# Kernel tuning notes

Hardware: AMD Instinct MI355X
Metric: run time of the kernel (lower is better)

Reference implementation:

```python
import jax, jax.numpy as jnp
import numpy as np

VOCAB = 30522
HIDDEN = 768
MAX_POS = 512
TYPE_VOCAB = 2
EPS = 1e-5


def setup_inputs() -> dict:
    key = jax.random.key(0)
    k1, k2, k3, k4, k5 = jax.random.split(key, 5)
    B, S = 32, 512
    return {
        "input_ids": jax.random.randint(k1, (B, S), 0, VOCAB, dtype=jnp.int64 if jax.config.jax_enable_x64 else jnp.int32),
        "token_type_ids": jax.random.randint(k2, (B, S), 0, TYPE_VOCAB, dtype=jnp.int32),
        "tok_w": jax.random.normal(k3, (VOCAB, HIDDEN), dtype=jnp.float32),
        "pos_w": jax.random.normal(k4, (MAX_POS, HIDDEN), dtype=jnp.float32),
        "type_w": jax.random.normal(k5, (TYPE_VOCAB, HIDDEN), dtype=jnp.float32),
        "gamma": jnp.ones((HIDDEN,), dtype=jnp.float32),
        "beta": jnp.zeros((HIDDEN,), dtype=jnp.float32),
    }


def reference(input_ids, token_type_ids, tok_w, pos_w, type_w, gamma, beta):
    S = input_ids.shape[-1]
    # One-hot-matmul lookups are mathematically plain gathers.
    emb = tok_w[input_ids] + pos_w[jnp.arange(S)] + type_w[token_type_ids]  # [B,S,H]
    mean = jnp.mean(emb, axis=-1, keepdims=True)
    var = jnp.mean(jnp.square(emb - mean), axis=-1, keepdims=True)  # unbiased=False
    out = (emb - mean) * gamma * jax.lax.rsqrt(var + EPS) + beta
    return out  # dropout p=0.0 (eval) is identity
```

## Files before the change

kernel.cpp:

```cpp
#include <hip/hip_runtime.h>

#define HIDDEN 768
#define LN_EPS 1e-5f

typedef float f32x4 __attribute__((ext_vector_type(4)));

__global__ __launch_bounds__(256) void bert_embedding_kernel(
    const int* __restrict__ input_ids,
    const int* __restrict__ token_type_ids,
    const float* __restrict__ tok_w,
    const float* __restrict__ pos_w,
    const float* __restrict__ type_w,
    const float* __restrict__ gamma,
    const float* __restrict__ beta,
    float* __restrict__ out,
    int n_rows, int S)
{
    const int wave = (blockIdx.x * blockDim.x + threadIdx.x) >> 6;
    const int lane = threadIdx.x & 63;
    if (wave >= n_rows) return;

    const int s = wave % S;
    const int tok = input_ids[wave];
    const int typ = token_type_ids[wave];

    const f32x4* __restrict__ tw = reinterpret_cast<const f32x4*>(tok_w  + (size_t)tok * HIDDEN);
    const f32x4* __restrict__ pw = reinterpret_cast<const f32x4*>(pos_w  + (size_t)s   * HIDDEN);
    const f32x4* __restrict__ yw = reinterpret_cast<const f32x4*>(type_w + (size_t)typ * HIDDEN);

    f32x4 e[3];
    float sum = 0.f, sumsq = 0.f;
    #pragma unroll
    for (int k = 0; k < 3; ++k) {
        const int idx = lane + k * 64;
        const f32x4 a = tw[idx];
        const f32x4 b = pw[idx];
        const f32x4 c = yw[idx];
        f32x4 v = a + b + c;
        e[k] = v;
        sum   += v.x + v.y + v.z + v.w;
        sumsq += v.x * v.x + v.y * v.y + v.z * v.z + v.w * v.w;
    }

    #pragma unroll
    for (int m = 1; m < 64; m <<= 1) {
        sum   += __shfl_xor(sum, m);
        sumsq += __shfl_xor(sumsq, m);
    }

    const float inv_h = 1.0f / (float)HIDDEN;
    const float mean = sum * inv_h;
    const float var  = sumsq * inv_h - mean * mean;
    const float rs   = rsqrtf(var + LN_EPS);

    f32x4* __restrict__ o = reinterpret_cast<f32x4*>(out + (size_t)wave * HIDDEN);
    const f32x4* __restrict__ g4 = reinterpret_cast<const f32x4*>(gamma);
    const f32x4* __restrict__ b4 = reinterpret_cast<const f32x4*>(beta);

    #pragma unroll
    for (int k = 0; k < 3; ++k) {
        const int idx = lane + k * 64;
        const f32x4 g  = g4[idx];
        const f32x4 bb = b4[idx];
        const f32x4 v  = e[k];
        f32x4 r;
        r.x = (v.x - mean) * rs * g.x + bb.x;
        r.y = (v.y - mean) * rs * g.y + bb.y;
        r.z = (v.z - mean) * rs * g.z + bb.z;
        r.w = (v.w - mean) * rs * g.w + bb.w;
        __builtin_nontemporal_store(r, &o[idx]);
    }
}

extern "C" void kernel_launch(void* const* d_in, const int* in_sizes, int n_in,
                              void* d_out, int out_size, void* d_ws, size_t ws_size,
                              hipStream_t stream) {
    const int*   input_ids      = (const int*)d_in[0];
    const int*   token_type_ids = (const int*)d_in[1];
    const float* tok_w          = (const float*)d_in[2];
    const float* pos_w          = (const float*)d_in[3];
    const float* type_w         = (const float*)d_in[4];
    const float* gamma          = (const float*)d_in[5];
    const float* beta           = (const float*)d_in[6];
    float* out = (float*)d_out;

    const int n_rows = in_sizes[0];
    const int S = in_sizes[3] / HIDDEN;

    const int waves_per_block = 4;
    const int blocks = (n_rows + waves_per_block - 1) / waves_per_block;
    bert_embedding_kernel<<<blocks, 256, 0, stream>>>(
        input_ids, token_type_ids, tok_w, pos_w, type_w, gamma, beta,
        out, n_rows, S);
}
```

Measured before the change: 21.01 us.

## Use persistent grid-stride waves with double-buffered row prefetch

Switches from one wave per row to a capped grid of waves that walk rows in a grid-stride loop. Each wave loads the next row's token, position and type embeddings while it normalizes the current one, and gamma/beta are loaded once per wave and kept in registers. The aim is to hide gather latency and cut per-row setup cost. The price is higher register pressure from two sets of buffers, and lower occupancy or fewer rows in flight per CU than the launch-everything approach.

After: 21.95 us. 1.04x slower.

```diff
diff --git a/kernel.cpp b/kernel.cpp
--- a/kernel.cpp
+++ b/kernel.cpp
@@ -16,59 +16,83 @@
     float* __restrict__ out,
     int n_rows, int S)
 {
+    const int lane = threadIdx.x & 63;
     const int wave = (blockIdx.x * blockDim.x + threadIdx.x) >> 6;
-    const int lane = threadIdx.x & 63;
+    const int NW   = (gridDim.x * blockDim.x) >> 6;
     if (wave >= n_rows) return;
 
-    const int s = wave % S;
-    const int tok = input_ids[wave];
-    const int typ = token_type_ids[wave];
+    const int i0 = lane, i1 = lane + 64, i2 = lane + 128;
 
-    const f32x4* __restrict__ tw = reinterpret_cast<const f32x4*>(tok_w  + (size_t)tok * HIDDEN);
-    const f32x4* __restrict__ pw = reinterpret_cast<const f32x4*>(pos_w  + (size_t)s   * HIDDEN);
-    const f32x4* __restrict__ yw = reinterpret_cast<const f32x4*>(type_w + (size_t)typ * HIDDEN);
-
-    f32x4 e[3];
-    float sum = 0.f, sumsq = 0.f;
-    #pragma unroll
-    for (int k = 0; k < 3; ++k) {
-        const int idx = lane + k * 64;
-        const f32x4 a = tw[idx];
-        const f32x4 b = pw[idx];
-        const f32x4 c = yw[idx];
-        f32x4 v = a + b + c;
-        e[k] = v;
-        sum   += v.x + v.y + v.z + v.w;
-        sumsq += v.x * v.x + v.y * v.y + v.z * v.z + v.w * v.w;
-    }
-
-    #pragma unroll
-    for (int m = 1; m < 64; m <<= 1) {
-        sum   += __shfl_xor(sum, m);
-        sumsq += __shfl_xor(sumsq, m);
-    }
-
-    const float inv_h = 1.0f / (float)HIDDEN;
-    const float mean = sum * inv_h;
-    const float var  = sumsq * inv_h - mean * mean;
-    const float rs   = rsqrtf(var + LN_EPS);
-
-    f32x4* __restrict__ o = reinterpret_cast<f32x4*>(out + (size_t)wave * HIDDEN);
     const f32x4* __restrict__ g4 = reinterpret_cast<const f32x4*>(gamma);
     const f32x4* __restrict__ b4 = reinterpret_cast<const f32x4*>(beta);
+    const f32x4 g0 = g4[i0], g1 = g4[i1], g2 = g4[i2];
+    const f32x4 bb0 = b4[i0], bb1 = b4[i1], bb2 = b4[i2];
 
-    #pragma unroll
-    for (int k = 0; k < 3; ++k) {
-        const int idx = lane + k * 64;
-        const f32x4 g  = g4[idx];
-        const f32x4 bb = b4[idx];
-        const f32x4 v  = e[k];
-        f32x4 r;
-        r.x = (v.x - mean) * rs * g.x + bb.x;
-        r.y = (v.y - mean) * rs * g.y + bb.y;
-        r.z = (v.z - mean) * rs * g.z + bb.z;
-        r.w = (v.w - mean) * rs * g.w + bb.w;
-        __builtin_nontemporal_store(r, &o[idx]);
+    auto LOAD = [&](int r, f32x4* a, f32x4* p, f32x4* c) {
+        const int tok = input_ids[r];
+        const int typ = token_type_ids[r];
+        const int s   = r % S;
+        const f32x4* __restrict__ tw = reinterpret_cast<const f32x4*>(tok_w  + (size_t)tok * HIDDEN);
+        const f32x4* __restrict__ pw = reinterpret_cast<const f32x4*>(pos_w  + (size_t)s   * HIDDEN);
+        const f32x4* __restrict__ yw = reinterpret_cast<const f32x4*>(type_w + (size_t)typ * HIDDEN);
+        a[0] = tw[i0]; a[1] = tw[i1]; a[2] = tw[i2];
+        p[0] = pw[i0]; p[1] = pw[i1]; p[2] = pw[i2];
+        c[0] = yw[i0]; c[1] = yw[i1]; c[2] = yw[i2];
+    };
+
+    auto PROCESS = [&](int r, const f32x4* a, const f32x4* p, const f32x4* c) {
+        const f32x4 e0 = a[0] + p[0] + c[0];
+        const f32x4 e1 = a[1] + p[1] + c[1];
+        const f32x4 e2 = a[2] + p[2] + c[2];
+        float sum = e0.x + e0.y + e0.z + e0.w
+                  + e1.x + e1.y + e1.z + e1.w
+                  + e2.x + e2.y + e2.z + e2.w;
+        float sq  = e0.x*e0.x + e0.y*e0.y + e0.z*e0.z + e0.w*e0.w
+                  + e1.x*e1.x + e1.y*e1.y + e1.z*e1.z + e1.w*e1.w
+                  + e2.x*e2.x + e2.y*e2.y + e2.z*e2.z + e2.w*e2.w;
+        #pragma unroll
+        for (int m = 1; m < 64; m <<= 1) {
+            sum += __shfl_xor(sum, m);
+            sq  += __shfl_xor(sq, m);
+        }
+        const float inv_h = 1.0f / (float)HIDDEN;
+        const float mean = sum * inv_h;
+        const float rs   = rsqrtf(sq * inv_h - mean * mean + LN_EPS);
+
+        f32x4* __restrict__ o = reinterpret_cast<f32x4*>(out + (size_t)r * HIDDEN);
+        f32x4 r0, r1, r2;
+        r0.x = (e0.x - mean) * rs * g0.x + bb0.x;
+        r0.y = (e0.y - mean) * rs * g0.y + bb0.y;
+        r0.z = (e0.z - mean) * rs * g0.z + bb0.z;
+        r0.w = (e0.w - mean) * rs * g0.w + bb0.w;
+        r1.x = (e1.x - mean) * rs * g1.x + bb1.x;
+        r1.y = (e1.y - mean) * rs * g1.y + bb1.y;
+        r1.z = (e1.z - mean) * rs * g1.z + bb1.z;
+        r1.w = (e1.w - mean) * rs * g1.w + bb1.w;
+        r2.x = (e2.x - mean) * rs * g2.x + bb2.x;
+        r2.y = (e2.y - mean) * rs * g2.y + bb2.y;
+        r2.z = (e2.z - mean) * rs * g2.z + bb2.z;
+        r2.w = (e2.w - mean) * rs * g2.w + bb2.w;
+        __builtin_nontemporal_store(r0, &o[i0]);
+        __builtin_nontemporal_store(r1, &o[i1]);
+        __builtin_nontemporal_store(r2, &o[i2]);
+    };
+
+    f32x4 aA[3], pA[3], cA[3];
+    f32x4 aB[3], pB[3], cB[3];
+
+    int rA = wave;
+    LOAD(rA, aA, pA, cA);
+    int rB = rA + NW;
+    while (true) {
+        if (rB < n_rows) LOAD(rB, aB, pB, cB);
+        PROCESS(rA, aA, pA, cA);
+        rA = rB + NW;
+        if (rB >= n_rows) break;
+        if (rA < n_rows) LOAD(rA, aA, pA, cA);
+        PROCESS(rB, aB, pB, cB);
+        rB = rA + NW;
+        if (rA >= n_rows) break;
     }
 }
 
@@ -87,8 +111,10 @@
     const int n_rows = in_sizes[0];
     const int S = in_sizes[3] / HIDDEN;
 
-    const int waves_per_block = 4;
-    const int blocks = (n_rows + waves_per_block - 1) / waves_per_block;
+    int waves_needed = (n_rows + 1) / 2;
+    int blocks = (waves_needed + 3) / 4;
+    if (blocks > 2048) blocks = 2048;
+    if (blocks < 1) blocks = 1;
     bert_embedding_kernel<<<blocks, 256, 0, stream>>>(
         input_ids, token_type_ids, tok_w, pos_w, type_w, gamma, beta,
         out, n_rows, S);
```
